# Performance work log

Hardware: AMD Instinct MI355X
Metric: run time of the kernel (lower is better)

## Reference

```python
import jax, jax.numpy as jnp
import numpy as np

IMG_H = IMG_W = 800
SIZES = (32, 64, 128, 256, 512)
FEAT_SHAPES = ((200, 200), (100, 100), (50, 50), (25, 25), (13, 13))
ASPECTS = np.array([0.5, 1.0, 2.0], np.float32)
MIN_SIZE = 10.0 / 1000.0
PRE_NMS = 4000
POST_NMS = 1000
IOU_TH = 0.7


def conv2d(x, w, b, pad):
    y = jax.lax.conv_general_dilated(
        x, w, window_strides=(1, 1), padding=[(pad, pad), (pad, pad)],
        dimension_numbers=("NCHW", "OIHW", "NCHW"))
    return y + b[None, :, None, None]


def make_anchors():
    # replicates torchvision AnchorGenerator: per-level single size, 3 aspect ratios
    out = []
    for (gh, gw), s in zip(FEAT_SHAPES, SIZES):
        h_r = np.sqrt(ASPECTS)
        w_r = 1.0 / h_r
        ws = s * w_r
        hs = s * h_r
        base = np.round(np.stack([-ws, -hs, ws, hs], 1) / 2.0)  # [3,4]
        stride_h = IMG_H // gh
        stride_w = IMG_W // gw
        sy = np.arange(gh, dtype=np.float32) * stride_h
        sx = np.arange(gw, dtype=np.float32) * stride_w
        yy, xx = np.meshgrid(sy, sx, indexing="ij")
        shifts = np.stack([xx, yy, xx, yy], axis=-1).reshape(-1, 1, 4)
        out.append((shifts + base[None]).reshape(-1, 4))
    a = np.concatenate(out, 0).astype(np.float32)
    a /= np.array([IMG_W, IMG_H, IMG_W, IMG_H], np.float32)  # normalize to [0,1]
    return jnp.asarray(a)


def xy_to_cxcy(a):
    return jnp.concatenate([(a[:, 2:] + a[:, :2]) / 2, a[:, 2:] - a[:, :2]], 1)


def cxcy_to_xy(a):
    return jnp.concatenate([a[:, :2] - a[:, 2:] / 2, a[:, :2] + a[:, 2:] / 2], 1)


def decode(t, anc):
    return jnp.concatenate([t[:, :2] * anc[:, 2:] + anc[:, :2],
                            jnp.exp(t[:, 2:]) * anc[:, 2:]], 1)


def rpn_head(feat, w_i, b_i, w_c, b_c, w_r, b_r):
    B = feat.shape[0]
    h = jax.nn.relu(conv2d(feat, w_i, b_i, 1))
    c = conv2d(h, w_c, b_c, 0).transpose(0, 2, 3, 1).reshape(B, -1, 2)
    r = conv2d(h, w_r, b_r, 0).transpose(0, 2, 3, 1).reshape(B, -1, 4)
    return c, r


def pairwise_iou(b):
    # b: [N,4] xyxy
    area = jnp.clip(b[:, 2] - b[:, 0], 0) * jnp.clip(b[:, 3] - b[:, 1], 0)
    lt = jnp.maximum(b[:, None, :2], b[None, :, :2])
    rb = jnp.minimum(b[:, None, 2:], b[None, :, 2:])
    wh = jnp.clip(rb - lt, 0)
    inter = wh[..., 0] * wh[..., 1]
    union = area[:, None] + area[None, :] - inter
    return jnp.where(union > 0, inter / union, 0.0)


def greedy_nms(ious, init_keep):
    N = ious.shape[0]
    idxs = jnp.arange(N)

    def body(i, keep):
        sup = keep[i] & (ious[i] > IOU_TH) & (idxs > i)
        return keep & ~sup

    return jax.lax.fori_loop(0, N, body, init_keep)


def rpn_forward(x, feats, w_inter, b_inter, w_cls, b_cls, w_reg, b_reg):
    cls_l, reg_l = [], []
    for f in feats:
        c, r = rpn_head(f, w_inter, b_inter, w_cls, b_cls, w_reg, b_reg)
        cls_l.append(c)
        reg_l.append(r)
    pred_cls = jnp.concatenate(cls_l, 1).reshape(-1, 2)   # [A,2]
    pred_reg = jnp.concatenate(reg_l, 1).reshape(-1, 4)   # [A,4]

    anchor = make_anchors()                               # [A,4] xyxy in [0,1]
    scores = jax.nn.softmax(pred_cls, axis=-1)[:, 1]
    roi = cxcy_to_xy(decode(pred_reg, xy_to_cxcy(anchor))).clip(0.0, 1.0)

    ws = roi[:, 2] - roi[:, 0]
    hs = roi[:, 3] - roi[:, 1]
    valid = (hs >= MIN_SIZE) & (ws >= MIN_SIZE)
    scores = jnp.where(valid, scores, -jnp.inf)

    top_scores, top_idx = jax.lax.top_k(scores, PRE_NMS)
    boxes = roi[top_idx]
    finite = jnp.isfinite(top_scores)
    boxes = jnp.where(finite[:, None], boxes, 0.0)  # neutralize filtered boxes

    ious = pairwise_iou(boxes)
    keep = greedy_nms(ious, finite)
    order = jnp.argsort(jnp.where(keep, jnp.arange(PRE_NMS), PRE_NMS + jnp.arange(PRE_NMS)))
    n_keep = jnp.minimum(keep.sum(), POST_NMS)
    sel = boxes[order[:POST_NMS]]
    roi_out = jnp.where(jnp.arange(POST_NMS)[:, None] < n_keep, sel, 0.0)  # padded [1000,4]
    return pred_cls, pred_reg, roi_out, anchor


def setup_inputs() -> dict:
    key = jax.random.key(0)
    ks = jax.random.split(key, 10)
    inp = {"x": jax.random.normal(ks[0], (1, 3, IMG_H, IMG_W), jnp.float32)}
    for i, (gh, gw) in enumerate(FEAT_SHAPES):
        inp[f"feat{i}"] = jax.random.normal(ks[1 + i], (1, 256, gh, gw), jnp.float32)
    # normal_init(m, 0, 0.01)
    inp["w_inter"] = jax.random.normal(ks[6], (256, 256, 3, 3), jnp.float32) * 0.01
    inp["b_inter"] = jnp.zeros((256,), jnp.float32)
    inp["w_cls"] = jax.random.normal(ks[7], (6, 256, 1, 1), jnp.float32) * 0.01
    inp["b_cls"] = jnp.zeros((6,), jnp.float32)
    inp["w_reg"] = jax.random.normal(ks[8], (12, 256, 1, 1), jnp.float32) * 0.01
    inp["b_reg"] = jnp.zeros((12,), jnp.float32)
    return inp


def reference(x, feat0, feat1, feat2, feat3, feat4,
              w_inter, b_inter, w_cls, b_cls, w_reg, b_reg):
    feats = [feat0, feat1, feat2, feat3, feat4]
    return rpn_forward(x, feats, w_inter, b_inter, w_cls, b_cls, w_reg, b_reg)
```

## Files before the change

kernel.cpp:

```cpp
#include <hip/hip_runtime.h>
#include <cmath>
#include <cstdint>

typedef unsigned int u32;
typedef unsigned long long u64;
typedef float v2f __attribute__((ext_vector_type(2)));

#define A_TOT   159882
#define PRE_NMS 4000
#define POST_NMS 1000
#define NWORDS  63
#define HIST_BINS 131072
#define HIST2_BINS 32768
#define SURV_CAP 8192
#define MONO_NEG_INF 0x007FFFFFu

struct BaseTab { float v[60]; };

__device__ inline u32 mono32f(float s) {
    u32 u = __float_as_uint(s);
    return (u & 0x80000000u) ? ~u : (u | 0x80000000u);
}

__device__ inline float pexp_f(float x0) {
    float x = fminf(x0, 88.3762626647950f);
    x = fmaxf(x, -88.3762626647949f);
    float m = floorf(__builtin_fmaf(x, 1.44269504088896341f, 0.5f));
    float r = __builtin_fmaf(m, -0.693359375f, x);
    r = __builtin_fmaf(m, 2.12194440e-4f, r);
    float z = r * r;
    float y = 1.9875691500E-4f;
    y = __builtin_fmaf(y, r, 1.3981999507E-3f);
    y = __builtin_fmaf(y, r, 8.3334519073E-3f);
    y = __builtin_fmaf(y, r, 4.1665795894E-2f);
    y = __builtin_fmaf(y, r, 1.6666665459E-1f);
    y = __builtin_fmaf(y, r, 5.0000001201E-1f);
    y = __builtin_fmaf(y, z, r);
    y = y + 1.0f;
    return ldexpf(y, (int)m);
}

__device__ inline float4 decode_box(const float* __restrict__ reg,
                                    const float* __restrict__ anc,
                                    u32 i, bool* valid) {
#pragma clang fp contract(off)
    float x1 = anc[4 * i], y1 = anc[4 * i + 1], x2 = anc[4 * i + 2], y2 = anc[4 * i + 3];
    float acx = (x2 + x1) / 2.0f, acy = (y2 + y1) / 2.0f;
    float aw = x2 - x1, ah = y2 - y1;
    float t0 = reg[4 * i], t1 = reg[4 * i + 1], t2 = reg[4 * i + 2], t3 = reg[4 * i + 3];
    float cx = (t0 * aw) + acx;
    float cy = (t1 * ah) + acy;
    float w  = pexp_f(t2) * aw;
    float hh = pexp_f(t3) * ah;
    float bx1 = fminf(fmaxf(cx - w / 2.0f, 0.f), 1.f);
    float by1 = fminf(fmaxf(cy - hh / 2.0f, 0.f), 1.f);
    float bx2 = fminf(fmaxf(cx + w / 2.0f, 0.f), 1.f);
    float by2 = fminf(fmaxf(cy + hh / 2.0f, 0.f), 1.f);
    float wsz = bx2 - bx1, hsz = by2 - by1;
    *valid = (hsz >= 0.01f) && (wsz >= 0.01f);
    return make_float4(bx1, by1, bx2, by2);
}

__device__ inline v2f pk_mul_blo(v2f a, v2f b) {
    v2f d;
    asm("v_pk_mul_f32 %0, %1, %2 op_sel:[0,0] op_sel_hi:[1,0]"
        : "=v"(d) : "v"(a), "v"(b));
    return d;
}
__device__ inline v2f pk_mul_bhi(v2f a, v2f b) {
    v2f d;
    asm("v_pk_mul_f32 %0, %1, %2 op_sel:[0,1] op_sel_hi:[1,1]"
        : "=v"(d) : "v"(a), "v"(b));
    return d;
}
__device__ inline v2f pk_add(v2f a, v2f b) {
    v2f d;
    asm("v_pk_add_f32 %0, %1, %2" : "=v"(d) : "v"(a), "v"(b));
    return d;
}

__device__ inline void gload16(const float* g, void* lds) {
    __builtin_amdgcn_global_load_lds(
        (const __attribute__((address_space(1))) void*)g,
// ... 102 lines not shown
    const int sfirst = pb * 9;
    ISSUE_X(sfirst);
    COMMIT_X(0);
    ISSUE_W(sfirst, 0);
    ISSUE_X(sfirst + 1);
    __syncthreads();
    int cur = 0;

    for (int pi = pb; pi < pb + npan; ++pi) {
        v2f pA0=(v2f)0.f, pA1=(v2f)0.f, pA2=(v2f)0.f, pA3=(v2f)0.f;
        v2f pB0=(v2f)0.f, pB1=(v2f)0.f, pB2=(v2f)0.f, pB3=(v2f)0.f;
        for (int j = 0; j < 9; ++j) {
            int s = pi * 9 + j;
            int nxt = cur ^ 1;
            bool more = (s + 1 < send);
            if (more) {
                COMMIT_X(nxt);
                ISSUE_W(s + 1, nxt);
                if (s + 2 < send) ISSUE_X(s + 2);
            }
            const float* Wb = &Ws[cur][0][0];
            const float* Xb = &Xs[cur][0][0];
#pragma unroll 4
            for (int kk = 0; kk < 32; ++kk) {
                float4 xv = *(const float4*)(Xb + kk * 32 + xg * 4);
                v2f xlo; xlo[0] = xv.x; xlo[1] = xv.y;
                v2f xhi; xhi[0] = xv.z; xhi[1] = xv.w;
                v2f wA = *(const v2f*)(Wb + kk * 128 + cg * 2);
                pA0 = pk_add(pA0, pk_mul_blo(wA, xlo));
                pA1 = pk_add(pA1, pk_mul_bhi(wA, xlo));
                pA2 = pk_add(pA2, pk_mul_blo(wA, xhi));
                pA3 = pk_add(pA3, pk_mul_bhi(wA, xhi));
                v2f wB = *(const v2f*)(Wb + kk * 128 + 64 + cg * 2);
                pB0 = pk_add(pB0, pk_mul_blo(wB, xlo));
                pB1 = pk_add(pB1, pk_mul_bhi(wB, xlo));
                pB2 = pk_add(pB2, pk_mul_blo(wB, xhi));
                pB3 = pk_add(pB3, pk_mul_bhi(wB, xhi));
            }
            if (more) {
                __syncthreads();
                cur = nxt;
            }
        }
        tA0 = pk_add(tA0, pA0); tA1 = pk_add(tA1, pA1);
        tA2 = pk_add(tA2, pA2); tA3 = pk_add(tA3, pA3);
        tB0 = pk_add(tB0, pB0); tB1 = pk_add(tB1, pB1);
        tB2 = pk_add(tB2, pB2); tB3 = pk_add(tB3, pB3);
    }
#undef ISSUE_X
#undef COMMIT_X
#undef ISSUE_W
    const int c0 = z2 * 128 + cg * 2;
    if (cm.fuse[l]) {
        const float* bias = cm.bias;
        float bA0 = bias[c0], bA1 = bias[c0 + 1];
        float bB0 = bias[c0 + 64], bB1 = bias[c0 + 65];
        tA0[0] = fmaxf(tA0[0] + bA0, 0.f); tA0[1] = fmaxf(tA0[1] + bA1, 0.f);
        tA1[0] = fmaxf(tA1[0] + bA0, 0.f); tA1[1] = fmaxf(tA1[1] + bA1, 0.f);
        tA2[0] = fmaxf(tA2[0] + bA0, 0.f); tA2[1] = fmaxf(tA2[1] + bA1, 0.f);
        tA3[0] = fmaxf(tA3[0] + bA0, 0.f); tA3[1] = fmaxf(tA3[1] + bA1, 0.f);
        tB0[0] = fmaxf(tB0[0] + bB0, 0.f); tB0[1] = fmaxf(tB0[1] + bB1, 0.f);
        tB1[0] = fmaxf(tB1[0] + bB0, 0.f); tB1[1] = fmaxf(tB1[1] + bB1, 0.f);
        tB2[0] = fmaxf(tB2[0] + bB0, 0.f); tB2[1] = fmaxf(tB2[1] + bB1, 0.f);
        tB3[0] = fmaxf(tB3[0] + bB0, 0.f); tB3[1] = fmaxf(tB3[1] + bB1, 0.f);
    }
    float* op = part + (size_t)pslot * 256 * S;
    {
        int sp = s0 + xg * 4;
        size_t rA0 = (size_t)c0 * S + sp;
        size_t rA1 = rA0 + S;
        if (sp + 0 < S) { op[rA0 + 0] = tA0[0]; op[rA1 + 0] = tA0[1]; }
        if (sp + 1 < S) { op[rA0 + 1] = tA1[0]; op[rA1 + 1] = tA1[1]; }
        if (sp + 2 < S) { op[rA0 + 2] = tA2[0]; op[rA1 + 2] = tA2[1]; }
        if (sp + 3 < S) { op[rA0 + 3] = tA3[0]; op[rA1 + 3] = tA3[1]; }
        size_t rB0 = rA0 + (size_t)64 * S;
        size_t rB1 = rB0 + S;
        if (sp + 0 < S) { op[rB0 + 0] = tB0[0]; op[rB1 + 0] = tB0[1]; }
        if (sp + 1 < S) { op[rB0 + 1] = tB1[0]; op[rB1 + 1] = tB1[1]; }
        if (sp + 2 < S) { op[rB0 + 2] = tB2[0]; op[rB1 + 2] = tB2[1]; }
        if (sp + 3 < S) { op[rB0 + 3] = tB3[0]; op[rB1 + 3] = tB3[1]; }
    }
}

struct HeadMap {
    const float* h[5];
    int S[5], abase[5], npan[5], bstart[6];
};

__global__ __launch_bounds__(256) void head_all(
    HeadMap hm, const float* __restrict__ wc,
    const float* __restrict__ bc, const float* __restrict__ wr,
    const float* __restrict__ br, const float* __restrict__ bias,
    float* __restrict__ cls_out, float* __restrict__ reg_out)
{
#pragma clang fp contract(off)
    int bid = blockIdx.x;
    int l = (bid >= hm.bstart[1]) + (bid >= hm.bstart[2]) +
            (bid >= hm.bstart[3]) + (bid >= hm.bstart[4]);
    int local = bid - hm.bstart[l];
    const float* __restrict__ h = hm.h[l];
    const int S = hm.S[l];
    const int abase = hm.abase[l];
    const int npan = hm.npan[l];
    int s = local * 256 + threadIdx.x;
    if (s >= S) return;
    float ac[6]  = {0.f};
    float ar[12] = {0.f};
    for (int c = 0; c < 256; ++c) {
        size_t i = (size_t)c * S + s;
        float v;
        if (npan == 1) {
            v = h[i];
        } else {
            float vv = h[i];
            for (int p = 1; p < 8; ++p)
                vv = vv + h[(size_t)p * 256 * S + i];
            v = fmaxf(vv + bias[c], 0.f);
        }
#pragma unroll
        for (int ch = 0; ch < 6; ++ch) {
            float prod = wc[ch * 256 + c] * v;
            ac[ch] = ac[ch] + prod;
        }
#pragma unroll
        for (int ch = 0; ch < 12; ++ch) {
            float prod = wr[ch * 256 + c] * v;
            ar[ch] = ar[ch] + prod;
        }
    }
    long b2 = (long)abase + (long)s * 3;
#pragma unroll
    for (int a = 0; a < 3; ++a) {
#pragma unroll
        for (int c2 = 0; c2 < 2; ++c2)
            cls_out[(b2 + a) * 2 + c2] = ac[a * 2 + c2] + bc[a * 2 + c2];
#pragma unroll
        for (int d = 0; d < 4; ++d)
            reg_out[(b2 + a) * 4 + d] = ar[a * 4 + d] + br[a * 4 + d];
    }
}

__global__ __launch_bounds__(256) void score_k(
    const float* __restrict__ cls, const float* __restrict__ reg,
    BaseTab bt, u64* __restrict__ keys, u32* __restrict__ hist,
    float* __restrict__ anc_out)
{
#pragma clang fp contract(off)
    int i = blockIdx.x * 256 + threadIdx.x;
    if (i >= A_TOT) return;
    int l, base, gw, str;
    if (i < 120000)      { l = 0; base = 0;      gw = 200; str = 4;  }
    else if (i < 150000) { l = 1; base = 120000; gw = 100; str = 8;  }
    else if (i < 157500) { l = 2; base = 150000; gw = 50;  str = 16; }
    else if (i < 159375) { l = 3; base = 157500; gw = 25;  str = 32; }
    else                 { l = 4; base = 159375; gw = 13;  str = 61; }
    int j = i - base;
    int sj = j / 3;
    int a = j - sj * 3;
    int yy = sj / gw;
    int xx = sj - yy * gw;
    float sx = (float)(xx * str), sy = (float)(yy * str);
    const float* bb = &bt.v[(l * 3 + a) * 4];
    float a0 = (sx + bb[0]) / 800.0f;
    float a1 = (sy + bb[1]) / 800.0f;
    float a2 = (sx + bb[2]) / 800.0f;
    float a3 = (sy + bb[3]) / 800.0f;
    anc_out[4 * i + 0] = a0;
    anc_out[4 * i + 1] = a1;
    anc_out[4 * i + 2] = a2;
    anc_out[4 * i + 3] = a3;
    float l0 = cls[2 * i], l1 = cls[2 * i + 1];
    float m  = fmaxf(l0, l1);
    float e0 = pexp_f(l0 - m);
    float e1 = pexp_f(l1 - m);
    float sum = e0 + e1;
    float sc  = e1 / sum;
    float acx = (a2 + a0) / 2.0f, acy = (a3 + a1) / 2.0f;
    float aw = a2 - a0, ah = a3 - a1;
    float t0 = reg[4 * i], t1 = reg[4 * i + 1], t2 = reg[4 * i + 2], t3 = reg[4 * i + 3];
    float cx = (t0 * aw) + acx;
    float cy = (t1 * ah) + acy;
    float w  = pexp_f(t2) * aw;
    float hh = pexp_f(t3) * ah;
    float bx1 = fminf(fmaxf(cx - w / 2.0f, 0.f), 1.f);
    float by1 = fminf(fmaxf(cy - hh / 2.0f, 0.f), 1.f);
    float bx2 = fminf(fmaxf(cx + w / 2.0f, 0.f), 1.f);
    float by2 = fminf(fmaxf(cy + hh / 2.0f, 0.f), 1.f);
    float wsz = bx2 - bx1, hsz = by2 - by1;
    bool valid = (hsz >= 0.01f) && (wsz >= 0.01f);

    float score = valid ? sc : -INFINITY;
    u32 u = mono32f(score);
    keys[i] = ((u64)u << 32) | (u32)(~(u32)i);
    atomicAdd(&hist[u >> 15], 1u);
}

__global__ __launch_bounds__(1024) void topk_thresh(const u32* __restrict__ hist,
                                                    u32* __restrict__ counters) {
    __shared__ u32 part[1024];
    int t = threadIdx.x;
    u32 s = 0;
    for (int q = 0; q < 128; ++q) s += hist[HIST_BINS - 1 - (t * 128 + q)];
    part[t] = s;
    __syncthreads();
    if (t == 0) {
        u32 cum = 0, cumBefore = 0;
        int tc = 1023;
        for (int c = 0; c < 1024; ++c) {
            if (cum + part[c] >= PRE_NMS) { tc = c; cumBefore = cum; break; }
            cum += part[c];
        }
        u32 cum2 = cumBefore;
        int bstar = 0;
        for (int q = 0; q < 128; ++q) {
            int b = HIST_BINS - 1 - (tc * 128 + q);
            u32 hv = hist[b];
            if (cum2 + hv >= PRE_NMS) { bstar = b; break; }
            cum2 += hv;
        }
        counters[0] = (u32)bstar;
        counters[1] = cum2;
    }
}

__global__ __launch_bounds__(256) void hist2_k(const u64* __restrict__ keys,
                                               const u32* __restrict__ counters,
                                               u32* __restrict__ hist2) {
    int i = blockIdx.x * 256 + threadIdx.x;
    if (i >= A_TOT) return;
    u32 u = (u32)(keys[i] >> 32);
    if ((u >> 15) == counters[0]) atomicAdd(&hist2[u & 0x7FFF], 1u);
}

__global__ __launch_bounds__(1024) void thresh2_k(const u32* __restrict__ hist2,
                                                  u32* __restrict__ counters) {
    __shared__ u32 part[1024];
    int t = threadIdx.x;
    u32 s = 0;
    for (int q = 0; q < 32; ++q) s += hist2[HIST2_BINS - 1 - (t * 32 + q)];
    part[t] = s;
    __syncthreads();
    if (t == 0) {
        u32 bstar = counters[0];
        u32 cum = counters[1];
        int tc = 1023;
        u32 cumBefore = cum;
        for (int c = 0; c < 1024; ++c) {
            if (cum + part[c] >= PRE_NMS) { tc = c; cumBefore = cum; break; }
            cum += part[c];
        }
        u32 cum2 = cumBefore;
        u32 low = 0;
        for (int q = 0; q < 32; ++q) {
            int b = HIST2_BINS - 1 - (tc * 32 + q);
            u32 hv = hist2[b];
            if (cum2 + hv >= PRE_NMS) { low = (u32)b; break; }
            cum2 += hv;
        }
        counters[3] = (bstar << 15) | low;
    }
}

__global__ __launch_bounds__(256) void compact_k(const u64* __restrict__ keys,
                                                 u32* __restrict__ counters,
                                                 u64* __restrict__ surv) {
    int i = blockIdx.x * 256 + threadIdx.x;
    if (i >= A_TOT) return;
    u32 cut = counters[3];
    u64 k = keys[i];
    if ((u32)(k >> 32) >= cut) {
        u32 slot = atomicAdd(&counters[2], 1u);
        if (slot < SURV_CAP) surv[slot] = k;
    }
}

__global__ __launch_bounds__(1024) void sort_topk(
    const u64* __restrict__ surv, const u32* __restrict__ counters,
    const float* __restrict__ reg, const float* __restrict__ anc,
    float* __restrict__ boxes4k, u64* __restrict__ finmask)
{
    __shared__ u64 K[SURV_CAP];
    int t = threadIdx.x;
    u32 n = counters[2];
    if (n > SURV_CAP) n = SURV_CAP;
    for (int p = t; p < SURV_CAP; p += 1024) K[p] = (p < (int)n) ? surv[p] : 0ull;
    __syncthreads();
    for (int k = 2; k <= SURV_CAP; k <<= 1) {
        for (int j = k >> 1; j > 0; j >>= 1) {
            for (int p = t; p < SURV_CAP / 2; p += 1024) {
                int i = 2 * p - (p & (j - 1));
                int pr = i + j;
                bool desc = ((i & k) == 0);
                u64 a = K[i], b = K[pr];
                if (desc ? (a < b) : (a > b)) { K[i] = b; K[pr] = a; }
            }
            __syncthreads();
        }
    }
    for (int jj = t; jj < PRE_NMS; jj += 1024) {
        u64 key = K[jj];
        u32 u = (u32)(key >> 32);
        float b0 = 0.f, b1 = 0.f, b2 = 0.f, b3 = 0.f;
        if (u > MONO_NEG_INF) {
            u32 idx = ~(u32)key;
            bool valid;
            float4 bx = decode_box(reg, anc, idx, &valid);
            b0 = bx.x; b1 = bx.y; b2 = bx.z; b3 = bx.w;
        }
        boxes4k[4 * jj + 0] = b0;
        boxes4k[4 * jj + 1] = b1;
        boxes4k[4 * jj + 2] = b2;
        boxes4k[4 * jj + 3] = b3;
    }
    if (t < NWORDS) {
        u64 wmask = 0;
        for (int b = 0; b < 64; ++b) {
            int jj = t * 64 + b;
            if (jj < PRE_NMS) {
                u32 u = (u32)(K[jj] >> 32);
                if (u > MONO_NEG_INF) wmask |= (1ull << b);
            }
        }
        finmask[t] = wmask;
    }
}

__global__ __launch_bounds__(64) void supmat_k(const float* __restrict__ boxes4k,
                                               u64* __restrict__ sup) {
#pragma clang fp contract(off)
    __shared__ float cb[64][4];
    int rb = blockIdx.y, cbk = blockIdx.x;
    int tl = threadIdx.x;
    int j = cbk * 64 + tl;
    if (j < PRE_NMS) {
        cb[tl][0] = boxes4k[4 * j + 0];
        cb[tl][1] = boxes4k[4 * j + 1];
        cb[tl][2] = boxes4k[4 * j + 2];
        cb[tl][3] = boxes4k[4 * j + 3];
    } else {
        cb[tl][0] = cb[tl][1] = cb[tl][2] = cb[tl][3] = 0.f;
    }
    __syncthreads();
    int i = rb * 64 + tl;
    if (i >= PRE_NMS) return;
    float ax1 = boxes4k[4 * i + 0], ay1 = boxes4k[4 * i + 1];
    float ax2 = boxes4k[4 * i + 2], ay2 = boxes4k[4 * i + 3];
    float aarea = fmaxf(ax2 - ax1, 0.f) * fmaxf(ay2 - ay1, 0.f);
    u64 w = 0;
    for (int q = 0; q < 64; ++q) {
        int jg = cbk * 64 + q;
        if (jg >= PRE_NMS || jg <= i) continue;
        float bx1 = cb[q][0], by1 = cb[q][1], bx2 = cb[q][2], by2 = cb[q][3];
        float barea = fmaxf(bx2 - bx1, 0.f) * fmaxf(by2 - by1, 0.f);
        float lx = fmaxf(ax1, bx1), ly = fmaxf(ay1, by1);
        float rx = fminf(ax2, bx2), ry = fminf(ay2, by2);
        float iw = fmaxf(rx - lx, 0.f), ih = fmaxf(ry - ly, 0.f);
        float inter = iw * ih;
        float uni = (aarea + barea) - inter;
        float iou = (uni > 0.f) ? inter / uni : 0.f;
        if (iou > 0.7f) w |= (1ull << q);
    }
    sup[(size_t)i * NWORDS + cbk] = w;
}

__device__ inline u64 shfl_u64(u64 v, int lane) {
    int lo = __shfl((int)(u32)(v & 0xFFFFFFFFull), lane, 64);
    int hi = __shfl((int)(u32)(v >> 32), lane, 64);
    return ((u64)(u32)hi << 32) | (u32)lo;
}

__global__ __launch_bounds__(64) void nms_scan_k(const u64* __restrict__ sup,
                                                 const u64* __restrict__ finmask,
                                                 u64* __restrict__ keepw) {
    int lane = threadIdx.x;
    u64 keep = (lane < NWORDS) ? finmask[lane] : 0ull;
    u64 cur[8], nxt[8];
#pragma unroll
    for (int q = 0; q < 8; ++q)
        cur[q] = (lane < NWORDS) ? sup[(size_t)q * NWORDS + lane] : 0ull;
    for (int base = 0; base < PRE_NMS; base += 8) {
        int nb = base + 8;
#pragma unroll
        for (int q = 0; q < 8; ++q) {
            int i = nb + q;
            nxt[q] = (lane < NWORDS && i < PRE_NMS) ? sup[(size_t)i * NWORDS + lane] : 0ull;
        }
#pragma unroll
        for (int q = 0; q < 8; ++q) {
            int i = base + q;
            int wi = i >> 6, bi = i & 63;
            u64 kw = shfl_u64(keep, wi);
            if ((kw >> bi) & 1ull) keep &= ~cur[q];
        }
#pragma unroll
        for (int q = 0; q < 8; ++q) cur[q] = nxt[q];
    }
    if (lane < NWORDS) keepw[lane] = keep;
}

__global__ __launch_bounds__(1024) void output_k(const u64* __restrict__ keepw,
                                                 const float* __restrict__ boxes4k,
                                                 float* __restrict__ roi_out) {
    __shared__ u32 pref[NWORDS + 1];
    int t = threadIdx.x;
    if (t == 0) {
        u32 run = 0;
        for (int w = 0; w < NWORDS; ++w) { pref[w] = run; run += (u32)__popcll(keepw[w]); }
        pref[NWORDS] = run;
    }
    __syncthreads();
    u32 total = pref[NWORDS];
    u32 nk = total < (u32)POST_NMS ? total : (u32)POST_NMS;
    for (int j = t; j < PRE_NMS; j += 1024) {
        int wi = j >> 6, bi = j & 63;
        u64 kw = keepw[wi];
        if ((kw >> bi) & 1ull) {
            u32 rank = pref[wi] + (u32)__popcll(kw & ((1ull << bi) - 1ull));
            if (rank < (u32)POST_NMS) {
                roi_out[4 * rank + 0] = boxes4k[4 * j + 0];
                roi_out[4 * rank + 1] = boxes4k[4 * j + 1];
                roi_out[4 * rank + 2] = boxes4k[4 * j + 2];
                roi_out[4 * rank + 3] = boxes4k[4 * j + 3];
            }
        }
    }
    for (int r2 = t; r2 < POST_NMS; r2 += 1024) {
        if ((u32)r2 >= nk) {
            roi_out[4 * r2 + 0] = 0.f;
            roi_out[4 * r2 + 1] = 0.f;
            roi_out[4 * r2 + 2] = 0.f;
            roi_out[4 * r2 + 3] = 0.f;
        }
    }
}

extern "C" void kernel_launch(void* const* d_in, const int* in_sizes, int n_in,
                              void* d_out, int out_size, void* d_ws, size_t ws_size,
                              hipStream_t stream) {
    const float* feat[5] = {
        (const float*)d_in[1], (const float*)d_in[2], (const float*)d_in[3],
        (const float*)d_in[4], (const float*)d_in[5]};
    const float* w_inter = (const float*)d_in[6];
    const float* b_inter = (const float*)d_in[7];
    const float* w_cls   = (const float*)d_in[8];
    const float* b_cls   = (const float*)d_in[9];
    const float* w_reg   = (const float*)d_in[10];
    const float* b_reg   = (const float*)d_in[11];

    float* out     = (float*)d_out;
    float* out_cls = out;
    float* out_reg = out + 319764;
    float* out_roi = out + 959292;
    float* out_anc = out + 963292;

    static const int GH[5]    = {200, 100, 50, 25, 13};
    static const int GW[5]    = {200, 100, 50, 25, 13};
    static const int SL[5]    = {40000, 10000, 2500, 625, 169};
    static const int ABASE[5] = {0, 120000, 150000, 157500, 159375};
    static const int NPAN_ST[5] = {1, 1, 8, 8, 8};

    char* p = (char*)d_ws;
    size_t off = 0;
    auto alloc = [&](size_t bytes) -> void* {
        void* r = p + off;
        off = (off + bytes + 255) & ~(size_t)255;
        return r;
    };
    float* Wt      = (float*)alloc((size_t)2304 * 256 * 4);
    float* part[5];
    for (int l = 0; l < 5; ++l)
        part[l] = (float*)alloc((size_t)NPAN_ST[l] * 256 * SL[l] * 4);
    u64*   keys    = (u64*)  alloc((size_t)A_TOT * 8);
    u32*   hist    = (u32*)  alloc((size_t)HIST_BINS * 4);
    u32*   hist2   = (u32*)  alloc((size_t)HIST2_BINS * 4);
    u32*   counters= (u32*)  alloc(256);
    u64*   surv    = (u64*)  alloc((size_t)SURV_CAP * 8);
    float* boxes4k = (float*)alloc((size_t)PRE_NMS * 4 * 4);
    u64*   finmask = (u64*)  alloc(64 * 8);
    u64*   supmat  = (u64*)  alloc((size_t)PRE_NMS * NWORDS * 8);
    u64*   keepw   = (u64*)  alloc(64 * 8);
    (void)ws_size;

    BaseTab bt;
    {
        const float sizes[5] = {32.f, 64.f, 128.f, 256.f, 512.f};
        const float asp[3] = {0.5f, 1.0f, 2.0f};
        for (int l = 0; l < 5; ++l)
            for (int a = 0; a < 3; ++a) {
                float hr = sqrtf(asp[a]);
                float wr = 1.0f / hr;
                float wsf = sizes[l] * wr;
                float hsf = sizes[l] * hr;
                bt.v[(l * 3 + a) * 4 + 0] = rintf(-wsf / 2.0f);
                bt.v[(l * 3 + a) * 4 + 1] = rintf(-hsf / 2.0f);
                bt.v[(l * 3 + a) * 4 + 2] = rintf( wsf / 2.0f);
                bt.v[(l * 3 + a) * 4 + 3] = rintf( hsf / 2.0f);
            }
    }

    hipMemsetAsync(hist, 0, (size_t)HIST_BINS * 4, stream);
    hipMemsetAsync(hist2, 0, (size_t)HIST2_BINS * 4, stream);
    hipMemsetAsync(counters, 0, 256, stream);

    wt_k<<<2304, 256, 0, stream>>>(w_inter, Wt);

    ConvMap cm;
    cm.Wt = Wt;
    cm.bias = b_inter;
    int bacc = 0;
    for (int l = 0; l < 5; ++l) {
        cm.feat[l] = feat[l];
        cm.part[l] = part[l];
        int st = (SL[l] + 31) / 32;
        cm.st[l] = st; cm.gh[l] = GH[l]; cm.gw[l] = GW[l]; cm.S[l] = SL[l];
        cm.M[l] = (((u64)1 << 48) + (u64)GW[l] - 1) / (u64)GW[l];
        int zsplit = NPAN_ST[l];
        cm.npan[l] = (zsplit == 1) ? 8 : 1;
        cm.fuse[l] = (zsplit == 1) ? 1 : 0;
        cm.bstart[l] = bacc;
        bacc += st * (zsplit * 2);
    }
    cm.bstart[5] = bacc;
    conv_all<<<bacc, 256, 0, stream>>>(cm);

    HeadMap hm;
    int hacc = 0;
    for (int l = 0; l < 5; ++l) {
        hm.h[l] = part[l];
        hm.S[l] = SL[l];
        hm.abase[l] = ABASE[l];
        hm.npan[l] = NPAN_ST[l];
        hm.bstart[l] = hacc;
        hacc += (SL[l] + 255) / 256;
    }
    hm.bstart[5] = hacc;
    head_all<<<hacc, 256, 0, stream>>>(hm, w_cls, b_cls, w_reg, b_reg,
                                       b_inter, out_cls, out_reg);

    int nbA = (A_TOT + 255) / 256;
    score_k<<<nbA, 256, 0, stream>>>(out_cls, out_reg, bt, keys, hist, out_anc);
    topk_thresh<<<1, 1024, 0, stream>>>(hist, counters);
    hist2_k<<<nbA, 256, 0, stream>>>(keys, counters, hist2);
    thresh2_k<<<1, 1024, 0, stream>>>(hist2, counters);
    compact_k<<<nbA, 256, 0, stream>>>(keys, counters, surv);
    sort_topk<<<1, 1024, 0, stream>>>(surv, counters, out_reg, out_anc, boxes4k, finmask);
    supmat_k<<<dim3(NWORDS, NWORDS), 64, 0, stream>>>(boxes4k, supmat);
    nms_scan_k<<<1, 64, 0, stream>>>(supmat, finmask, keepw);
    output_k<<<1, 1024, 0, stream>>>(keepw, boxes4k, out_roi);
}
```

Before: 2.472 ms.

## Fuse post-conv pipeline into two cooperative kernels with grid syncs

Replaces the chain of small kernels (head, score, two histogram/threshold passes, compaction, sort, suppression matrix, NMS scan, output) and three memsets with two cooperative launches that use grid-wide syncs between phases. Histogram clearing moves into the first cooperative kernel, and the suppression matrix work is reorganised so each 256-thread block computes several column words. The goal is to remove per-launch overhead and gaps between many tiny dependent kernels. In exchange, the grids are limited to co-resident sizes, some phases run on a single block while the rest wait at grid barriers, and grid.sync itself has a cost.

```diff
diff --git a/kernel.cpp b/kernel.cpp
--- a/kernel.cpp
+++ b/kernel.cpp
@@ -1,4 +1,5 @@
 #include <hip/hip_runtime.h>
+#include <hip/hip_cooperative_groups.h>
 #include <cmath>
 #include <cstdint>
 
@@ -267,286 +268,204 @@
     }
 }
 
-struct HeadMap {
+struct Coop1Map {
     const float* h[5];
-    int S[5], abase[5], npan[5], bstart[6];
+    const float* wc; const float* bc; const float* wr; const float* br;
+    const float* bias;
+    float* cls_out; float* reg_out; float* anc_out;
+    u64* keys; u32* hist; u32* hist2; u32* counters; u64* surv;
+    BaseTab bt;
 };
 
-__global__ __launch_bounds__(256) void head_all(
-    HeadMap hm, const float* __restrict__ wc,
-    const float* __restrict__ bc, const float* __restrict__ wr,
-    const float* __restrict__ br, const float* __restrict__ bias,
-    float* __restrict__ cls_out, float* __restrict__ reg_out)
+__global__ __launch_bounds__(1024) void coop1(Coop1Map m)
 {
 #pragma clang fp contract(off)
-    int bid = blockIdx.x;
-    int l = (bid >= hm.bstart[1]) + (bid >= hm.bstart[2]) +
-            (bid >= hm.bstart[3]) + (bid >= hm.bstart[4]);
-    int local = bid - hm.bstart[l];
-    const float* __restrict__ h = hm.h[l];
-    const int S = hm.S[l];
-    const int abase = hm.abase[l];
-    const int npan = hm.npan[l];
-    int s = local * 256 + threadIdx.x;
-    if (s >= S) return;
-    float ac[6]  = {0.f};
-    float ar[12] = {0.f};
-    for (int c = 0; c < 256; ++c) {
-        size_t i = (size_t)c * S + s;
-        float v;
-        if (npan == 1) {
-            v = h[i];
-        } else {
-            float vv = h[i];
-            for (int p = 1; p < 8; ++p)
-                vv = vv + h[(size_t)p * 256 * S + i];
-            v = fmaxf(vv + bias[c], 0.f);
-        }
-#pragma unroll
-        for (int ch = 0; ch < 6; ++ch) {
-            float prod = wc[ch * 256 + c] * v;
-            ac[ch] = ac[ch] + prod;
-        }
-#pragma unroll
-        for (int ch = 0; ch < 12; ++ch) {
-            float prod = wr[ch * 256 + c] * v;
-            ar[ch] = ar[ch] + prod;
-        }
-    }
-    long b2 = (long)abase + (long)s * 3;
-#pragma unroll
-    for (int a = 0; a < 3; ++a) {
-#pragma unroll
-        for (int c2 = 0; c2 < 2; ++c2)
-            cls_out[(b2 + a) * 2 + c2] = ac[a * 2 + c2] + bc[a * 2 + c2];
-#pragma unroll
-        for (int d = 0; d < 4; ++d)
-            reg_out[(b2 + a) * 4 + d] = ar[a * 4 + d] + br[a * 4 + d];
-    }
-}
-
-__global__ __launch_bounds__(256) void score_k(
-    const float* __restrict__ cls, const float* __restrict__ reg,
-    BaseTab bt, u64* __restrict__ keys, u32* __restrict__ hist,
-    float* __restrict__ anc_out)
-{
-#pragma clang fp contract(off)
-    int i = blockIdx.x * 256 + threadIdx.x;
-    if (i >= A_TOT) return;
-    int l, base, gw, str;
-    if (i < 120000)      { l = 0; base = 0;      gw = 200; str = 4;  }
-    else if (i < 150000) { l = 1; base = 120000; gw = 100; str = 8;  }
-    else if (i < 157500) { l = 2; base = 150000; gw = 50;  str = 16; }
-    else if (i < 159375) { l = 3; base = 157500; gw = 25;  str = 32; }
-    else                 { l = 4; base = 159375; gw = 13;  str = 61; }
-    int j = i - base;
-    int sj = j / 3;
-    int a = j - sj * 3;
-    int yy = sj / gw;
-    int xx = sj - yy * gw;
-    float sx = (float)(xx * str), sy = (float)(yy * str);
-    const float* bb = &bt.v[(l * 3 + a) * 4];
-    float a0 = (sx + bb[0]) / 800.0f;
-    float a1 = (sy + bb[1]) / 800.0f;
-    float a2 = (sx + bb[2]) / 800.0f;
-    float a3 = (sy + bb[3]) / 800.0f;
-    anc_out[4 * i + 0] = a0;
-    anc_out[4 * i + 1] = a1;
-    anc_out[4 * i + 2] = a2;
-    anc_out[4 * i + 3] = a3;
-    float l0 = cls[2 * i], l1 = cls[2 * i + 1];
-    float m  = fmaxf(l0, l1);
-    float e0 = pexp_f(l0 - m);
-    float e1 = pexp_f(l1 - m);
-    float sum = e0 + e1;
-    float sc  = e1 / sum;
-    float acx = (a2 + a0) / 2.0f, acy = (a3 + a1) / 2.0f;
-    float aw = a2 - a0, ah = a3 - a1;
-    float t0 = reg[4 * i], t1 = reg[4 * i + 1], t2 = reg[4 * i + 2], t3 = reg[4 * i + 3];
-    float cx = (t0 * aw) + acx;
-    float cy = (t1 * ah) + acy;
-    float w  = pexp_f(t2) * aw;
-    float hh = pexp_f(t3) * ah;
-    float bx1 = fminf(fmaxf(cx - w / 2.0f, 0.f), 1.f);
-    float by1 = fminf(fmaxf(cy - hh / 2.0f, 0.f), 1.f);
-    float bx2 = fminf(fmaxf(cx + w / 2.0f, 0.f), 1.f);
-    float by2 = fminf(fmaxf(cy + hh / 2.0f, 0.f), 1.f);
-    float wsz = bx2 - bx1, hsz = by2 - by1;
-    bool valid = (hsz >= 0.01f) && (wsz >= 0.01f);
-
-    float score = valid ? sc : -INFINITY;
-    u32 u = mono32f(score);
-    keys[i] = ((u64)u << 32) | (u32)(~(u32)i);
-    atomicAdd(&hist[u >> 15], 1u);
-}
-
-__global__ __launch_bounds__(1024) void topk_thresh(const u32* __restrict__ hist,
-                                                    u32* __restrict__ counters) {
     __shared__ u32 part[1024];
-    int t = threadIdx.x;
-    u32 s = 0;
-    for (int q = 0; q < 128; ++q) s += hist[HIST_BINS - 1 - (t * 128 + q)];
-    part[t] = s;
-    __syncthreads();
-    if (t == 0) {
-        u32 cum = 0, cumBefore = 0;
-        int tc = 1023;
-        for (int c = 0; c < 1024; ++c) {
-            if (cum + part[c] >= PRE_NMS) { tc = c; cumBefore = cum; break; }
-            cum += part[c];
-        }
-        u32 cum2 = cumBefore;
-        int bstar = 0;
-        for (int q = 0; q < 128; ++q) {
-            int b = HIST_BINS - 1 - (tc * 128 + q);
-            u32 hv = hist[b];
-            if (cum2 + hv >= PRE_NMS) { bstar = b; break; }
-            cum2 += hv;
-        }
-        counters[0] = (u32)bstar;
-        counters[1] = cum2;
-    }
-}
-
-__global__ __launch_bounds__(256) void hist2_k(const u64* __restrict__ keys,
-                                               const u32* __restrict__ counters,
-                                               u32* __restrict__ hist2) {
-    int i = blockIdx.x * 256 + threadIdx.x;
-    if (i >= A_TOT) return;
-    u32 u = (u32)(keys[i] >> 32);
-    if ((u >> 15) == counters[0]) atomicAdd(&hist2[u & 0x7FFF], 1u);
-}
-
-__global__ __launch_bounds__(1024) void thresh2_k(const u32* __restrict__ hist2,
-                                                  u32* __restrict__ counters) {
-    __shared__ u32 part[1024];
-    int t = threadIdx.x;
-    u32 s = 0;
-    for (int q = 0; q < 32; ++q) s += hist2[HIST2_BINS - 1 - (t * 32 + q)];
-    part[t] = s;
-    __syncthreads();
-    if (t == 0) {
-        u32 bstar = counters[0];
-        u32 cum = counters[1];
-        int tc = 1023;
-        u32 cumBefore = cum;
-        for (int c = 0; c < 1024; ++c) {
-            if (cum + part[c] >= PRE_NMS) { tc = c; cumBefore = cum; break; }
-            cum += part[c];
-        }
-        u32 cum2 = cumBefore;
-        u32 low = 0;
-        for (int q = 0; q < 32; ++q) {
-            int b = HIST2_BINS - 1 - (tc * 32 + q);
-            u32 hv = hist2[b];
-            if (cum2 + hv >= PRE_NMS) { low = (u32)b; break; }
-            cum2 += hv;
-        }
-        counters[3] = (bstar << 15) | low;
-    }
-}
-
-__global__ __launch_bounds__(256) void compact_k(const u64* __restrict__ keys,
-                                                 u32* __restrict__ counters,
-                                                 u64* __restrict__ surv) {
-    int i = blockIdx.x * 256 + threadIdx.x;
-    if (i >= A_TOT) return;
-    u32 cut = counters[3];
-    u64 k = keys[i];
-    if ((u32)(k >> 32) >= cut) {
-        u32 slot = atomicAdd(&counters[2], 1u);
-        if (slot < SURV_CAP) surv[slot] = k;
-    }
-}
-
-__global__ __launch_bounds__(1024) void sort_topk(
-    const u64* __restrict__ surv, const u32* __restrict__ counters,
-    const float* __restrict__ reg, const float* __restrict__ anc,
-    float* __restrict__ boxes4k, u64* __restrict__ finmask)
-{
-    __shared__ u64 K[SURV_CAP];
-    int t = threadIdx.x;
-    u32 n = counters[2];
-    if (n > SURV_CAP) n = SURV_CAP;
-    for (int p = t; p < SURV_CAP; p += 1024) K[p] = (p < (int)n) ? surv[p] : 0ull;
-    __syncthreads();
-    for (int k = 2; k <= SURV_CAP; k <<= 1) {
-        for (int j = k >> 1; j > 0; j >>= 1) {
-            for (int p = t; p < SURV_CAP / 2; p += 1024) {
-                int i = 2 * p - (p & (j - 1));
-                int pr = i + j;
-                bool desc = ((i & k) == 0);
-                u64 a = K[i], b = K[pr];
-                if (desc ? (a < b) : (a > b)) { K[i] = b; K[pr] = a; }
-            }
-            __syncthreads();
-        }
-    }
-    for (int jj = t; jj < PRE_NMS; jj += 1024) {
-        u64 key = K[jj];
-        u32 u = (u32)(key >> 32);
-        float b0 = 0.f, b1 = 0.f, b2 = 0.f, b3 = 0.f;
-        if (u > MONO_NEG_INF) {
-            u32 idx = ~(u32)key;
-            bool valid;
-            float4 bx = decode_box(reg, anc, idx, &valid);
-            b0 = bx.x; b1 = bx.y; b2 = bx.z; b3 = bx.w;
-        }
-        boxes4k[4 * jj + 0] = b0;
-        boxes4k[4 * jj + 1] = b1;
-        boxes4k[4 * jj + 2] = b2;
-        boxes4k[4 * jj + 3] = b3;
-    }
-    if (t < NWORDS) {
-        u64 wmask = 0;
-        for (int b = 0; b < 64; ++b) {
-            int jj = t * 64 + b;
-            if (jj < PRE_NMS) {
-                u32 u = (u32)(K[jj] >> 32);
-                if (u > MONO_NEG_INF) wmask |= (1ull << b);
-            }
-        }
-        finmask[t] = wmask;
-    }
-}
-
-__global__ __launch_bounds__(64) void supmat_k(const float* __restrict__ boxes4k,
-                                               u64* __restrict__ sup) {
-#pragma clang fp contract(off)
-    __shared__ float cb[64][4];
-    int rb = blockIdx.y, cbk = blockIdx.x;
-    int tl = threadIdx.x;
-    int j = cbk * 64 + tl;
-    if (j < PRE_NMS) {
-        cb[tl][0] = boxes4k[4 * j + 0];
-        cb[tl][1] = boxes4k[4 * j + 1];
-        cb[tl][2] = boxes4k[4 * j + 2];
-        cb[tl][3] = boxes4k[4 * j + 3];
-    } else {
-        cb[tl][0] = cb[tl][1] = cb[tl][2] = cb[tl][3] = 0.f;
-    }
-    __syncthreads();
-    int i = rb * 64 + tl;
-    if (i >= PRE_NMS) return;
-    float ax1 = boxes4k[4 * i + 0], ay1 = boxes4k[4 * i + 1];
-    float ax2 = boxes4k[4 * i + 2], ay2 = boxes4k[4 * i + 3];
-    float aarea = fmaxf(ax2 - ax1, 0.f) * fmaxf(ay2 - ay1, 0.f);
-    u64 w = 0;
-    for (int q = 0; q < 64; ++q) {
-        int jg = cbk * 64 + q;
-        if (jg >= PRE_NMS || jg <= i) continue;
-        float bx1 = cb[q][0], by1 = cb[q][1], bx2 = cb[q][2], by2 = cb[q][3];
-        float barea = fmaxf(bx2 - bx1, 0.f) * fmaxf(by2 - by1, 0.f);
-        float lx = fmaxf(ax1, bx1), ly = fmaxf(ay1, by1);
-        float rx = fminf(ax2, bx2), ry = fminf(ay2, by2);
-        float iw = fmaxf(rx - lx, 0.f), ih = fmaxf(ry - ly, 0.f);
-        float inter = iw * ih;
-        float uni = (aarea + barea) - inter;
-        float iou = (uni > 0.f) ? inter / uni : 0.f;
-        if (iou > 0.7f) w |= (1ull << q);
-    }
-    sup[(size_t)i * NWORDS + cbk] = w;
-}
+    cooperative_groups::grid_group gg = cooperative_groups::this_grid();
+    const int t = threadIdx.x;
+    const int bid = blockIdx.x;
+    const int gid = bid * 1024 + t;
+    const int nthr = (int)gridDim.x * 1024;
+
+    if (gid < 53294) {
+        int s, S, abase, npan;
+        const float* h;
+        if (gid < 40000)      { s = gid;         S = 40000; abase = 0;      npan = 1; h = m.h[0]; }
+        else if (gid < 50000) { s = gid - 40000; S = 10000; abase = 120000; npan = 1; h = m.h[1]; }
+        else if (gid < 52500) { s = gid - 50000; S = 2500;  abase = 150000; npan = 8; h = m.h[2]; }
+        else if (gid < 53125) { s = gid - 52500; S = 625;   abase = 157500; npan = 8; h = m.h[3]; }
+        else                  { s = gid - 53125; S = 169;   abase = 159375; npan = 8; h = m.h[4]; }
+        float ac[6]  = {0.f};
+        float ar[12] = {0.f};
+        for (int c = 0; c < 256; ++c) {
+            size_t i = (size_t)c * S + s;
+            float v;
+            if (npan == 1) {
+                v = h[i];
+            } else {
+                float vv = h[i];
+                for (int p = 1; p < 8; ++p)
+                    vv = vv + h[(size_t)p * 256 * S + i];
+                v = fmaxf(vv + m.bias[c], 0.f);
+            }
+#pragma unroll
+            for (int ch = 0; ch < 6; ++ch) {
+                float prod = m.wc[ch * 256 + c] * v;
+                ac[ch] = ac[ch] + prod;
+            }
+#pragma unroll
+            for (int ch = 0; ch < 12; ++ch) {
+                float prod = m.wr[ch * 256 + c] * v;
+                ar[ch] = ar[ch] + prod;
+            }
+        }
+        long b2 = (long)abase + (long)s * 3;
+#pragma unroll
+        for (int a = 0; a < 3; ++a) {
+#pragma unroll
+            for (int c2 = 0; c2 < 2; ++c2)
+                m.cls_out[(b2 + a) * 2 + c2] = ac[a * 2 + c2] + m.bc[a * 2 + c2];
+#pragma unroll
+            for (int d = 0; d < 4; ++d)
+                m.reg_out[(b2 + a) * 4 + d] = ar[a * 4 + d] + m.br[a * 4 + d];
+        }
+    }
+    for (int i2 = gid; i2 < HIST_BINS; i2 += nthr) m.hist[i2] = 0;
+    for (int i2 = gid; i2 < HIST2_BINS; i2 += nthr) m.hist2[i2] = 0;
+    if (gid < 64) m.counters[gid] = 0;
+    __threadfence();
+    gg.sync();
+
+    if (gid < A_TOT) {
+        int i = gid;
+        int l, base, gw, str;
+        if (i < 120000)      { l = 0; base = 0;      gw = 200; str = 4;  }
+        else if (i < 150000) { l = 1; base = 120000; gw = 100; str = 8;  }
+        else if (i < 157500) { l = 2; base = 150000; gw = 50;  str = 16; }
+        else if (i < 159375) { l = 3; base = 157500; gw = 25;  str = 32; }
+        else                 { l = 4; base = 159375; gw = 13;  str = 61; }
+        int j = i - base;
+        int sj = j / 3;
+        int a = j - sj * 3;
+        int yy = sj / gw;
+        int xx = sj - yy * gw;
+        float sx = (float)(xx * str), sy = (float)(yy * str);
+        const float* bb = &m.bt.v[(l * 3 + a) * 4];
+        float a0 = (sx + bb[0]) / 800.0f;
+        float a1 = (sy + bb[1]) / 800.0f;
+        float a2 = (sx + bb[2]) / 800.0f;
+        float a3 = (sy + bb[3]) / 800.0f;
+        m.anc_out[4 * i + 0] = a0;
+        m.anc_out[4 * i + 1] = a1;
+        m.anc_out[4 * i + 2] = a2;
+        m.anc_out[4 * i + 3] = a3;
+        float l0 = m.cls_out[2 * i], l1 = m.cls_out[2 * i + 1];
+        float mm = fmaxf(l0, l1);
+        float e0 = pexp_f(l0 - mm);
+        float e1 = pexp_f(l1 - mm);
+        float sum = e0 + e1;
+        float sc  = e1 / sum;
+        float acx = (a2 + a0) / 2.0f, acy = (a3 + a1) / 2.0f;
+        float aw = a2 - a0, ah = a3 - a1;
+        float t0 = m.reg_out[4 * i], t1 = m.reg_out[4 * i + 1];
+        float t2 = m.reg_out[4 * i + 2], t3 = m.reg_out[4 * i + 3];
+        float cx = (t0 * aw) + acx;
+        float cy = (t1 * ah) + acy;
+        float w  = pexp_f(t2) * aw;
+        float hh = pexp_f(t3) * ah;
+        float bx1 = fminf(fmaxf(cx - w / 2.0f, 0.f), 1.f);
+        float by1 = fminf(fmaxf(cy - hh / 2.0f, 0.f), 1.f);
+        float bx2 = fminf(fmaxf(cx + w / 2.0f, 0.f), 1.f);
+        float by2 = fminf(fmaxf(cy + hh / 2.0f, 0.f), 1.f);
+        float wsz = bx2 - bx1, hsz = by2 - by1;
+        bool valid = (hsz >= 0.01f) && (wsz >= 0.01f);
+        float score = valid ? sc : -INFINITY;
+        u32 u = mono32f(score);
+        m.keys[i] = ((u64)u << 32) | (u32)(~(u32)i);
+        atomicAdd(&m.hist[u >> 15], 1u);
+    }
+    __threadfence();
+    gg.sync();
+
+    if (bid == 0) {
+        u32 s = 0;
+        for (int q = 0; q < 128; ++q) s += m.hist[HIST_BINS - 1 - (t * 128 + q)];
+        part[t] = s;
+        __syncthreads();
+        if (t == 0) {
+            u32 cum = 0, cumBefore = 0;
+            int tc = 1023;
+            for (int c = 0; c < 1024; ++c) {
+                if (cum + part[c] >= PRE_NMS) { tc = c; cumBefore = cum; break; }
+                cum += part[c];
+            }
+            u32 cum2 = cumBefore;
+            int bstar = 0;
+            for (int q = 0; q < 128; ++q) {
+                int b = HIST_BINS - 1 - (tc * 128 + q);
+                u32 hv = m.hist[b];
+                if (cum2 + hv >= PRE_NMS) { bstar = b; break; }
+                cum2 += hv;
+            }
+            m.counters[0] = (u32)bstar;
+            m.counters[1] = cum2;
+        }
+        __syncthreads();
+    }
+    __threadfence();
+    gg.sync();
+
+    if (gid < A_TOT) {
+        u32 u = (u32)(m.keys[gid] >> 32);
+        if ((u >> 15) == m.counters[0]) atomicAdd(&m.hist2[u & 0x7FFF], 1u);
+    }
+    __threadfence();
+    gg.sync();
+
+    if (bid == 0) {
+        u32 s = 0;
+        for (int q = 0; q < 32; ++q) s += m.hist2[HIST2_BINS - 1 - (t * 32 + q)];
+        part[t] = s;
+        __syncthreads();
+        if (t == 0) {
+            u32 bstar = m.counters[0];
+            u32 cum = m.counters[1];
+            int tc = 1023;
+            u32 cumBefore = cum;
+            for (int c = 0; c < 1024; ++c) {
+                if (cum + part[c] >= PRE_NMS) { tc = c; cumBefore = cum; break; }
+                cum += part[c];
+            }
+            u32 cum2 = cumBefore;
+            u32 low = 0;
+            for (int q = 0; q < 32; ++q) {
+                int b = HIST2_BINS - 1 - (tc * 32 + q);
+                u32 hv = m.hist2[b];
+                if (cum2 + hv >= PRE_NMS) { low = (u32)b; break; }
+                cum2 += hv;
+            }
+            m.counters[3] = (bstar << 15) | low;
+        }
+        __syncthreads();
+    }
+    __threadfence();
+    gg.sync();
+
+    if (gid < A_TOT) {
+        u32 cut = m.counters[3];
+        u64 k = m.keys[gid];
+        if ((u32)(k >> 32) >= cut) {
+            u32 slot = atomicAdd(&m.counters[2], 1u);
+            if (slot < SURV_CAP) m.surv[slot] = k;
+        }
+    }
+}
+
+struct Coop2Map {
+    const u64* surv; const u32* counters;
+    const float* reg; const float* anc;
+    float* boxes4k; u64* finmask; u64* sup; float* roi_out;
+};
 
 __device__ inline u64 shfl_u64(u64 v, int lane) {
     int lo = __shfl((int)(u32)(v & 0xFFFFFFFFull), lane, 64);
@@ -554,67 +473,169 @@
     return ((u64)(u32)hi << 32) | (u32)lo;
 }
 
-__global__ __launch_bounds__(64) void nms_scan_k(const u64* __restrict__ sup,
-                                                 const u64* __restrict__ finmask,
-                                                 u64* __restrict__ keepw) {
-    int lane = threadIdx.x;
-    u64 keep = (lane < NWORDS) ? finmask[lane] : 0ull;
-    u64 cur[8], nxt[8];
-#pragma unroll
-    for (int q = 0; q < 8; ++q)
-        cur[q] = (lane < NWORDS) ? sup[(size_t)q * NWORDS + lane] : 0ull;
-    for (int base = 0; base < PRE_NMS; base += 8) {
-        int nb = base + 8;
-#pragma unroll
-        for (int q = 0; q < 8; ++q) {
-            int i = nb + q;
-            nxt[q] = (lane < NWORDS && i < PRE_NMS) ? sup[(size_t)i * NWORDS + lane] : 0ull;
-        }
-#pragma unroll
-        for (int q = 0; q < 8; ++q) {
-            int i = base + q;
-            int wi = i >> 6, bi = i & 63;
-            u64 kw = shfl_u64(keep, wi);
-            if ((kw >> bi) & 1ull) keep &= ~cur[q];
-        }
-#pragma unroll
-        for (int q = 0; q < 8; ++q) cur[q] = nxt[q];
-    }
-    if (lane < NWORDS) keepw[lane] = keep;
-}
-
-__global__ __launch_bounds__(1024) void output_k(const u64* __restrict__ keepw,
-                                                 const float* __restrict__ boxes4k,
-                                                 float* __restrict__ roi_out) {
+__global__ __launch_bounds__(256) void coop2(Coop2Map m)
+{
+#pragma clang fp contract(off)
+    __shared__ u64 K[SURV_CAP];
+    __shared__ float cb[8][64][4];
+    __shared__ u64 keepw_s[NWORDS];
     __shared__ u32 pref[NWORDS + 1];
-    int t = threadIdx.x;
+    cooperative_groups::grid_group gg = cooperative_groups::this_grid();
+    const int t = threadIdx.x;
+    const int bid = blockIdx.x;
+
+    if (bid == 0) {
+        u32 n = m.counters[2];
+        if (n > SURV_CAP) n = SURV_CAP;
+        for (int p = t; p < SURV_CAP; p += 256) K[p] = (p < (int)n) ? m.surv[p] : 0ull;
+        __syncthreads();
+        for (int k = 2; k <= SURV_CAP; k <<= 1) {
+            for (int j = k >> 1; j > 0; j >>= 1) {
+                for (int p = t; p < SURV_CAP / 2; p += 256) {
+                    int i = 2 * p - (p & (j - 1));
+                    int pr = i + j;
+                    bool desc = ((i & k) == 0);
+                    u64 a = K[i], b = K[pr];
+                    if (desc ? (a < b) : (a > b)) { K[i] = b; K[pr] = a; }
+                }
+                __syncthreads();
+            }
+        }
+        for (int jj = t; jj < PRE_NMS; jj += 256) {
+            u64 key = K[jj];
+            u32 u = (u32)(key >> 32);
+            float b0 = 0.f, b1 = 0.f, b2 = 0.f, b3 = 0.f;
+            if (u > MONO_NEG_INF) {
+                u32 idx = ~(u32)key;
+                bool valid;
+                float4 bx = decode_box(m.reg, m.anc, idx, &valid);
+                b0 = bx.x; b1 = bx.y; b2 = bx.z; b3 = bx.w;
+            }
+            m.boxes4k[4 * jj + 0] = b0;
+            m.boxes4k[4 * jj + 1] = b1;
+            m.boxes4k[4 * jj + 2] = b2;
+            m.boxes4k[4 * jj + 3] = b3;
+        }
+        if (t < NWORDS) {
+            u64 wmask = 0;
+            for (int b = 0; b < 64; ++b) {
+                int jj = t * 64 + b;
+                if (jj < PRE_NMS) {
+                    u32 u = (u32)(K[jj] >> 32);
+                    if (u > MONO_NEG_INF) wmask |= (1ull << b);
+                }
+            }
+            m.finmask[t] = wmask;
+        }
+    }
+    __threadfence();
+    gg.sync();
+
+    {
+        int rb = bid >> 3, grp = bid & 7;
+        for (int e = t; e < 512; e += 256) {
+            int cc = e >> 6, q = e & 63;
+            int j = (grp * 8 + cc) * 64 + q;
+            if (j < PRE_NMS) {
+                cb[cc][q][0] = m.boxes4k[4 * j + 0];
+                cb[cc][q][1] = m.boxes4k[4 * j + 1];
+                cb[cc][q][2] = m.boxes4k[4 * j + 2];
+                cb[cc][q][3] = m.boxes4k[4 * j + 3];
+            } else {
+                cb[cc][q][0] = cb[cc][q][1] = cb[cc][q][2] = cb[cc][q][3] = 0.f;
+            }
+        }
+        __syncthreads();
+        int sub = t >> 6, tl = t & 63;
+        int i = rb * 64 + tl;
+        if (i < PRE_NMS) {
+            float ax1 = m.boxes4k[4 * i + 0], ay1 = m.boxes4k[4 * i + 1];
+            float ax2 = m.boxes4k[4 * i + 2], ay2 = m.boxes4k[4 * i + 3];
+            float aarea = fmaxf(ax2 - ax1, 0.f) * fmaxf(ay2 - ay1, 0.f);
+#pragma unroll
+            for (int it = 0; it < 2; ++it) {
+                int cc = it * 4 + sub;
+                int cbk = grp * 8 + cc;
+                if (cbk >= NWORDS) continue;
+                u64 w = 0;
+                for (int q = 0; q < 64; ++q) {
+                    int jg = cbk * 64 + q;
+                    if (jg >= PRE_NMS || jg <= i) continue;
+                    float bx1 = cb[cc][q][0], by1 = cb[cc][q][1];
+                    float bx2 = cb[cc][q][2], by2 = cb[cc][q][3];
+                    float barea = fmaxf(bx2 - bx1, 0.f) * fmaxf(by2 - by1, 0.f);
+                    float lx = fmaxf(ax1, bx1), ly = fmaxf(ay1, by1);
+                    float rx = fminf(ax2, bx2), ry = fminf(ay2, by2);
+                    float iw = fmaxf(rx - lx, 0.f), ih = fmaxf(ry - ly, 0.f);
+                    float inter = iw * ih;
+                    float uni = (aarea + barea) - inter;
+                    float iou = (uni > 0.f) ? inter / uni : 0.f;
+                    if (iou > 0.7f) w |= (1ull << q);
+                }
+                m.sup[(size_t)i * NWORDS + cbk] = w;
+            }
+        }
+    }
+    __threadfence();
+    gg.sync();
+
+    if (bid != 0) return;
+
+    if (t < 64) {
+        int lane = t;
+        u64 keep = (lane < NWORDS) ? m.finmask[lane] : 0ull;
+        u64 cur[8], nxt[8];
+#pragma unroll
+        for (int q = 0; q < 8; ++q)
+            cur[q] = (lane < NWORDS) ? m.sup[(size_t)q * NWORDS + lane] : 0ull;
+        for (int base = 0; base < PRE_NMS; base += 8) {
+            int nb = base + 8;
+#pragma unroll
+            for (int q = 0; q < 8; ++q) {
+                int i = nb + q;
+                nxt[q] = (lane < NWORDS && i < PRE_NMS) ? m.sup[(size_t)i * NWORDS + lane] : 0ull;
+            }
+#pragma unroll
+            for (int q = 0; q < 8; ++q) {
+                int i = base + q;
+                int wi = i >> 6, bi = i & 63;
+                u64 kw = shfl_u64(keep, wi);
+                if ((kw >> bi) & 1ull) keep &= ~cur[q];
+            }
+#pragma unroll
+            for (int q = 0; q < 8; ++q) cur[q] = nxt[q];
+        }
+        if (lane < NWORDS) keepw_s[lane] = keep;
+    }
+    __syncthreads();
+
     if (t == 0) {
         u32 run = 0;
-        for (int w = 0; w < NWORDS; ++w) { pref[w] = run; run += (u32)__popcll(keepw[w]); }
+        for (int w = 0; w < NWORDS; ++w) { pref[w] = run; run += (u32)__popcll(keepw_s[w]); }
         pref[NWORDS] = run;
     }
     __syncthreads();
     u32 total = pref[NWORDS];
     u32 nk = total < (u32)POST_NMS ? total : (u32)POST_NMS;
-    for (int j = t; j < PRE_NMS; j += 1024) {
+    for (int j = t; j < PRE_NMS; j += 256) {
         int wi = j >> 6, bi = j & 63;
-        u64 kw = keepw[wi];
+        u64 kw = keepw_s[wi];
         if ((kw >> bi) & 1ull) {
             u32 rank = pref[wi] + (u32)__popcll(kw & ((1ull << bi) - 1ull));
             if (rank < (u32)POST_NMS) {
-                roi_out[4 * rank + 0] = boxes4k[4 * j + 0];
-                roi_out[4 * rank + 1] = boxes4k[4 * j + 1];
-                roi_out[4 * rank + 2] = boxes4k[4 * j + 2];
-                roi_out[4 * rank + 3] = boxes4k[4 * j + 3];
-            }
-        }
-    }
-    for (int r2 = t; r2 < POST_NMS; r2 += 1024) {
+                m.roi_out[4 * rank + 0] = m.boxes4k[4 * j + 0];
+                m.roi_out[4 * rank + 1] = m.boxes4k[4 * j + 1];
+                m.roi_out[4 * rank + 2] = m.boxes4k[4 * j + 2];
+                m.roi_out[4 * rank + 3] = m.boxes4k[4 * j + 3];
+            }
+        }
+    }
+    for (int r2 = t; r2 < POST_NMS; r2 += 256) {
         if ((u32)r2 >= nk) {
-            roi_out[4 * r2 + 0] = 0.f;
-            roi_out[4 * r2 + 1] = 0.f;
-            roi_out[4 * r2 + 2] = 0.f;
-            roi_out[4 * r2 + 3] = 0.f;
+            m.roi_out[4 * r2 + 0] = 0.f;
+            m.roi_out[4 * r2 + 1] = 0.f;
+            m.roi_out[4 * r2 + 2] = 0.f;
+            m.roi_out[4 * r2 + 3] = 0.f;
         }
     }
 }
@@ -641,7 +662,6 @@
     static const int GH[5]    = {200, 100, 50, 25, 13};
     static const int GW[5]    = {200, 100, 50, 25, 13};
     static const int SL[5]    = {40000, 10000, 2500, 625, 169};
-    static const int ABASE[5] = {0, 120000, 150000, 157500, 159375};
     static const int NPAN_ST[5] = {1, 1, 8, 8, 8};
 
     char* p = (char*)d_ws;
@@ -663,7 +683,6 @@
     float* boxes4k = (float*)alloc((size_t)PRE_NMS * 4 * 4);
     u64*   finmask = (u64*)  alloc(64 * 8);
     u64*   supmat  = (u64*)  alloc((size_t)PRE_NMS * NWORDS * 8);
-    u64*   keepw   = (u64*)  alloc(64 * 8);
     (void)ws_size;
 
     BaseTab bt;
@@ -682,10 +701,6 @@
                 bt.v[(l * 3 + a) * 4 + 3] = rintf( hsf / 2.0f);
             }
     }
-
-    hipMemsetAsync(hist, 0, (size_t)HIST_BINS * 4, stream);
-    hipMemsetAsync(hist2, 0, (size_t)HIST2_BINS * 4, stream);
-    hipMemsetAsync(counters, 0, 256, stream);
 
     wt_k<<<2304, 256, 0, stream>>>(w_inter, Wt);
 
@@ -708,28 +723,26 @@
     cm.bstart[5] = bacc;
     conv_all<<<bacc, 256, 0, stream>>>(cm);
 
-    HeadMap hm;
-    int hacc = 0;
-    for (int l = 0; l < 5; ++l) {
-        hm.h[l] = part[l];
-        hm.S[l] = SL[l];
-        hm.abase[l] = ABASE[l];
-        hm.npan[l] = NPAN_ST[l];
-        hm.bstart[l] = hacc;
-        hacc += (SL[l] + 255) / 256;
-    }
-    hm.bstart[5] = hacc;
-    head_all<<<hacc, 256, 0, stream>>>(hm, w_cls, b_cls, w_reg, b_reg,
-                                       b_inter, out_cls, out_reg);
-
-    int nbA = (A_TOT + 255) / 256;
-    score_k<<<nbA, 256, 0, stream>>>(out_cls, out_reg, bt, keys, hist, out_anc);
-    topk_thresh<<<1, 1024, 0, stream>>>(hist, counters);
-    hist2_k<<<nbA, 256, 0, stream>>>(keys, counters, hist2);
-    thresh2_k<<<1, 1024, 0, stream>>>(hist2, counters);
-    compact_k<<<nbA, 256, 0, stream>>>(keys, counters, surv);
-    sort_topk<<<1, 1024, 0, stream>>>(surv, counters, out_reg, out_anc, boxes4k, finmask);
-    supmat_k<<<dim3(NWORDS, NWORDS), 64, 0, stream>>>(boxes4k, supmat);
-    nms_scan_k<<<1, 64, 0, stream>>>(supmat, finmask, keepw);
-    output_k<<<1, 1024, 0, stream>>>(keepw, boxes4k, out_roi);
-}
+    Coop1Map m1;
+    for (int l = 0; l < 5; ++l) m1.h[l] = part[l];
+    m1.wc = w_cls; m1.bc = b_cls; m1.wr = w_reg; m1.br = b_reg;
+    m1.bias = b_inter;
+    m1.cls_out = out_cls; m1.reg_out = out_reg; m1.anc_out = out_anc;
+    m1.keys = keys; m1.hist = hist; m1.hist2 = hist2; m1.counters = counters;
+    m1.surv = surv;
+    m1.bt = bt;
+    {
+        void* a1[] = { (void*)&m1 };
+        hipLaunchCooperativeKernel((void*)coop1, dim3(157), dim3(1024), a1, 0, stream);
+    }
+
+    Coop2Map m2;
+    m2.surv = surv; m2.counters = counters;
+    m2.reg = out_reg; m2.anc = out_anc;
+    m2.boxes4k = boxes4k; m2.finmask = finmask; m2.sup = supmat;
+    m2.roi_out = out_roi;
+    {
+        void* a2[] = { (void*)&m2 };
+        hipLaunchCooperativeKernel((void*)coop2, dim3(504), dim3(256), a2, 0, stream);
+    }
+}
```

Measured after the change: 2.998 ms. 21.3% more time.
